# Kernel optimization log

Hardware: AMD Instinct MI355X
Metric: run time of the kernel (lower is better)

Reference implementation:

```python
import jax, jax.numpy as jnp
import numpy as np

STRIDES = (8, 16, 32, 64, 128)
HS = (192, 96, 48, 24, 12)
NUM_CLASSES = 15
NUM_THETA = 18
B = 16
SCORE_THR = 0.05
IOU_THR = 0.3
MAX_DET = 1000


def setup_inputs() -> dict:
    key = jax.random.key(0)
    ks = jax.random.split(key, 20)
    inp = {}
    i = 0
    for name, c in (("cls", NUM_CLASSES), ("reg", 5), ("tc", NUM_THETA), ("tr", 1)):
        for l, h in enumerate(HS):
            inp[f"{name}_l{l}"] = jax.random.normal(ks[i], (B, c, h, h), dtype=jnp.float32)
            i += 1
    return inp


def _coords():
    # FCOS-style location centers per level, concatenated: [N, 2] (x, y)
    outs = []
    for h, s in zip(HS, STRIDES):
        c1d = jnp.arange(h, dtype=jnp.float32) * s + s // 2
        yy, xx = jnp.meshgrid(c1d, c1d, indexing="ij")
        outs.append(jnp.stack([xx.ravel(), yy.ravel()], axis=-1))
    return jnp.concatenate(outs, axis=0)


def _flatten(levels):
    # list of [B,C,h,w] -> [B, sum(h*w), C]  (permute to NHWC then reshape, as in torch)
    b = levels[0].shape[0]
    return jnp.concatenate(
        [jnp.transpose(t, (0, 2, 3, 1)).reshape(b, -1, t.shape[1]) for t in levels], axis=1
    )


def _pairwise_iou(boxes):
    # boxes [M,5] (x1,y1,x2,y2,theta); axis-aligned IoU on first 4 coords
    x1, y1, x2, y2 = boxes[:, 0], boxes[:, 1], boxes[:, 2], boxes[:, 3]
    area = jnp.clip(x2 - x1, 0.0) * jnp.clip(y2 - y1, 0.0)
    iw = jnp.clip(jnp.minimum(x2[:, None], x2[None, :]) - jnp.maximum(x1[:, None], x1[None, :]), 0.0)
    ih = jnp.clip(jnp.minimum(y2[:, None], y2[None, :]) - jnp.maximum(y1[:, None], y1[None, :]), 0.0)
    inter = iw * ih
    union = area[:, None] + area[None, :] - inter
    return inter / jnp.maximum(union, 1e-8)


def _nms_keep(boxes, valid, iou_thr):
    # greedy NMS over score-sorted boxes; returns bool keep mask [M]
    m = boxes.shape[0]
    iou = _pairwise_iou(boxes)
    idx = jnp.arange(m)

    def body(i, keep):
        sup = keep[i] & (iou[i] > iou_thr) & (idx > i)
        return keep & ~sup

    return jax.lax.fori_loop(0, m, body, valid)


def _forward(cls_levels, reg_levels, tc_levels, tr_levels):
    coords = _coords()  # [N,2]

    cls_preds = jax.nn.sigmoid(_flatten(cls_levels))          # [B,N,15]
    cls_scores = jnp.max(cls_preds, axis=-1)                   # [B,N]
    cls_classes = jnp.argmax(cls_preds, axis=-1) + 1           # [B,N]

    tc_preds = jax.nn.sigmoid(_flatten(tc_levels))             # [B,N,18]
    theta_c = (jnp.argmax(tc_preds, axis=-1) + 1)[..., None].astype(jnp.float32)  # [B,N,1]
    tr_lo = _flatten(tr_levels)                                # [B,N,1]
    theta = theta_c * 10.0 + tr_lo                             # [B,N,1]

    # reg: scale ltrb channels (0:4) by stride per level, keep angle channel raw
    reg_parts = []
    for t, s in zip(reg_levels, STRIDES):
        r = jnp.transpose(t, (0, 2, 3, 1)).reshape(t.shape[0], -1, 5)
        reg_parts.append(jnp.concatenate([r[..., :4] * float(s), r[..., 4:]], axis=-1))
    reg = jnp.concatenate(reg_parts, axis=1)                   # [B,N,5]

    x1y1 = coords[None, :, :] - reg[..., :2]
    x2y2 = coords[None, :, :] + reg[..., 2:4]
    boxes = jnp.concatenate([x1y1, x2y2, theta], axis=-1)      # [B,N,5]

    max_num = min(MAX_DET, cls_scores.shape[-1])
    top_scores, top_idx = jax.lax.top_k(cls_scores, max_num)   # sorted desc
    boxes_topk = jnp.take_along_axis(boxes, top_idx[..., None], axis=1)   # [B,M,5]
    classes_topk = jnp.take_along_axis(cls_classes, top_idx, axis=1)      # [B,M]

    valid = top_scores >= SCORE_THR
    keep = jax.vmap(lambda b, v: _nms_keep(b, v, IOU_THR))(boxes_topk, valid)  # [B,M] bool

    scores_post = top_scores * keep
    classes_post = classes_topk * keep
    boxes_post = boxes_topk * keep[..., None]
    return scores_post, classes_post, boxes_post


def reference(cls_l0, cls_l1, cls_l2, cls_l3, cls_l4,
              reg_l0, reg_l1, reg_l2, reg_l3, reg_l4,
              tc_l0, tc_l1, tc_l2, tc_l3, tc_l4,
              tr_l0, tr_l1, tr_l2, tr_l3, tr_l4):
    return _forward(
        [cls_l0, cls_l1, cls_l2, cls_l3, cls_l4],
        [reg_l0, reg_l1, reg_l2, reg_l3, reg_l4],
        [tc_l0, tc_l1, tc_l2, tc_l3, tc_l4],
        [tr_l0, tr_l1, tr_l2, tr_l3, tr_l4],
    )
```

## Files before the change

### kernel.cpp

```cpp
#include <hip/hip_runtime.h>
#include <stdint.h>

#define NCLS   15
#define NTH    18
#define BATCH  16
#define NANCH  49104
#define KTOP   1000
#define NWORDS 16
#define NBIN   32768
#define BSHIFT 15
#define CAND   2048

__device__ __forceinline__ float sigmoidf(float x) {
    return 1.0f / (1.0f + expf(-x));
}

__device__ __forceinline__ void levelOf(int i, int& lvl, int& h, int& s, int& pos) {
    if (i < 36864)      { lvl = 0; h = 192; s = 8;   pos = i; }
    else if (i < 46080) { lvl = 1; h = 96;  s = 16;  pos = i - 36864; }
    else if (i < 48384) { lvl = 2; h = 48;  s = 32;  pos = i - 46080; }
    else if (i < 48960) { lvl = 3; h = 24;  s = 64;  pos = i - 48384; }
    else                { lvl = 4; h = 12;  s = 128; pos = i - 48960; }
}

__device__ __forceinline__ unsigned long long shfl_u64(unsigned long long v, int src) {
    int lo = __shfl((int)(unsigned int)(v & 0xFFFFFFFFull), src);
    int hi = __shfl((int)(unsigned int)(v >> 32), src);
    return ((unsigned long long)(unsigned int)hi << 32) | (unsigned long long)(unsigned int)lo;
}

__device__ __forceinline__ void atomicOr64Shared(unsigned long long* p, unsigned long long v) {
    unsigned int* q = (unsigned int*)p;
    unsigned int lo = (unsigned int)v;
    unsigned int hi = (unsigned int)(v >> 32);
    if (lo) atomicOr(q, lo);
    if (hi) atomicOr(q + 1, hi);
}

__global__ __launch_bounds__(256) void k_scores(
    const float* __restrict__ c0, const float* __restrict__ c1,
    const float* __restrict__ c2, const float* __restrict__ c3,
    const float* __restrict__ c4,
    float* __restrict__ scores, unsigned char* __restrict__ classes,
    uint4* __restrict__ zero_region, int zero_n4)
{
    int g4 = blockIdx.x * 256 + threadIdx.x;
    if (g4 < zero_n4) zero_region[g4] = make_uint4(0u, 0u, 0u, 0u);
    if (g4 >= BATCH * NANCH / 4) return;
    int g = g4 * 4;
    int b = g / NANCH;
    int i = g - b * NANCH;
    int lvl, h, s, pos;
    levelOf(i, lvl, h, s, pos);
    int hh = h * h;
    const float* cp = (lvl == 0) ? c0 : (lvl == 1) ? c1 : (lvl == 2) ? c2
                      : (lvl == 3) ? c3 : c4;
    const float* base = cp + (size_t)b * NCLS * hh + pos;
    float4 best = make_float4(-1e30f, -1e30f, -1e30f, -1e30f);
    int bcx = 0, bcy = 0, bcz = 0, bcw = 0;
    #pragma unroll
    for (int c = 0; c < NCLS; ++c) {
        float4 v = *(const float4*)(base + (size_t)c * hh);
        float sx = sigmoidf(v.x), sy = sigmoidf(v.y);
        float sz = sigmoidf(v.z), sw = sigmoidf(v.w);
        if (sx > best.x) { best.x = sx; bcx = c; }
        if (sy > best.y) { best.y = sy; bcy = c; }
        if (sz > best.z) { best.z = sz; bcz = c; }
        if (sw > best.w) { best.w = sw; bcw = c; }
    }
    *(float4*)(scores + g) = best;
    *(uchar4*)(classes + g) = make_uchar4(
        (unsigned char)(bcx + 1), (unsigned char)(bcy + 1),
        (unsigned char)(bcz + 1), (unsigned char)(bcw + 1));
}

__global__ __launch_bounds__(256) void k_hist(
    const float* __restrict__ scores, unsigned int* __restrict__ hist)
{
    __shared__ unsigned int lh[NBIN / 2];
    const int b = blockIdx.y;
    for (int i = threadIdx.x; i < NBIN / 2; i += 256) lh[i] = 0u;
    __syncthreads();

    const float4* sv = (const float4*)(scores + (size_t)b * NANCH);
    for (int f4 = blockIdx.x * 256 + threadIdx.x; f4 < NANCH / 4; f4 += 6 * 256) {
        float4 v = sv[f4];
        unsigned int bin;
        bin = __float_as_uint(v.x) >> BSHIFT;
        atomicAdd(&lh[bin >> 1], 1u << ((bin & 1) << 4));
        bin = __float_as_uint(v.y) >> BSHIFT;
        atomicAdd(&lh[bin >> 1], 1u << ((bin & 1) << 4));
        bin = __float_as_uint(v.z) >> BSHIFT;
        atomicAdd(&lh[bin >> 1], 1u << ((bin & 1) << 4));
        bin = __float_as_uint(v.w) >> BSHIFT;
        atomicAdd(&lh[bin >> 1], 1u << ((bin & 1) << 4));
    }
    __syncthreads();

    unsigned int* hb = hist + (size_t)b * (NBIN / 2);
    for (int wd = threadIdx.x; wd < NBIN / 2; wd += 256) {
        unsigned int v = lh[wd];
        if (v) atomicAdd(&hb[wd], v);
    }
}

__global__ __launch_bounds__(256) void k_findT(
    const unsigned int* __restrict__ hist, int* __restrict__ tbin)
{
    int b = blockIdx.x;
    int tid = threadIdx.x;
    const unsigned int* hb = hist + (size_t)b * (NBIN / 2);
    __shared__ unsigned int sc[256];
    __shared__ unsigned int fsc[128];
    __shared__ int s_c, s_t;

    unsigned int s = 0;
    const uint4* hv = (const uint4*)(hb + (size_t)tid * 64);
    #pragma unroll 4
    for (int k = 0; k < 16; ++k) {
        uint4 v = hv[k];
        s += (v.x & 0xFFFFu) + (v.x >> 16) + (v.y & 0xFFFFu) + (v.y >> 16)
           + (v.z & 0xFFFFu) + (v.z >> 16) + (v.w & 0xFFFFu) + (v.w >> 16);
    }
    sc[tid] = s;
    if (tid == 0) { s_c = 0; s_t = 0; }
    __syncthreads();
    for (int d = 1; d < 256; d <<= 1) {
        unsigned int add = (tid + d < 256) ? sc[tid + d] : 0;
        __syncthreads();
        sc[tid] += add;
        __syncthreads();
    }
    if (sc[tid] >= (unsigned int)KTOP && (tid == 255 || sc[tid + 1] < (unsigned int)KTOP))
        s_c = tid;
    __syncthreads();
    int c = s_c;
    unsigned int hi = (c < 255) ? sc[c + 1] : 0;
    if (tid < 64) {
        unsigned int w = hb[c * 64 + tid];
        fsc[2 * tid]     = w & 0xFFFFu;
        fsc[2 * tid + 1] = w >> 16;
    }
    __syncthreads();
    for (int d = 1; d < 128; d <<= 1) {
        unsigned int add = (tid < 128 && tid + d < 128) ? fsc[tid + d] : 0;
        __syncthreads();
        if (tid < 128) fsc[tid] += add;
        __syncthreads();
    }
    if (tid < 128 && hi + fsc[tid] >= (unsigned int)KTOP &&
        (tid == 127 || hi + fsc[tid + 1] < (unsigned int)KTOP))
        s_t = tid;
    __syncthreads();
    if (tid == 0) tbin[b] = c * 128 + s_t;
}

__global__ __launch_bounds__(256) void k_compact(
    const float* __restrict__ scores, const int* __restrict__ tbin,
    int* __restrict__ cnt, unsigned long long* __restrict__ cand)
{
    const int b = blockIdx.y;
    const int t4 = blockIdx.x * 256 + threadIdx.x;
    __shared__ int lcnt;
    __shared__ int lbase;
    if (threadIdx.x == 0) lcnt = 0;
    __syncthreads();

    const int T = tbin[b];
    const bool in = (t4 < NANCH / 4);
    float4 v = make_float4(0.f, 0.f, 0.f, 0.f);
    if (in) v = *(const float4*)(scores + (size_t)b * NANCH + 4 * (size_t)t4);
    unsigned int bits[4] = { __float_as_uint(v.x), __float_as_uint(v.y),
                             __float_as_uint(v.z), __float_as_uint(v.w) };
    int rank[4];
    #pragma unroll
    for (int k = 0; k < 4; ++k) {
        bool pass = in && ((int)(bits[k] >> BSHIFT) >= T);
        rank[k] = pass ? atomicAdd(&lcnt, 1) : -1;
    }
    __syncthreads();
    if (threadIdx.x == 0) lbase = atomicAdd(&cnt[b * 16], lcnt);
    __syncthreads();
    const int base = lbase;
    #pragma unroll
    for (int k = 0; k < 4; ++k) {
        if (rank[k] >= 0) {
            int p = base + rank[k];
            if (p < CAND) {
                unsigned int idx = 4u * (unsigned int)t4 + (unsigned int)k;
                cand[(size_t)b * CAND + p] =
                    ((unsigned long long)bits[k] << 32) |
                    (unsigned long long)(0xFFFFFFFFu - idx);
            }
        }
    }
}

__global__ __launch_bounds__(256) void k_rankdec(
    const unsigned long long* __restrict__ cand, const int* __restrict__ cnt,
    const float* __restrict__ r0, const float* __restrict__ r1,
    const float* __restrict__ r2, const float* __restrict__ r3,
    const float* __restrict__ r4,
    const unsigned char* __restrict__ classes_all,
    float* __restrict__ tsc, int* __restrict__ tix,
    float* __restrict__ boxes, int* __restrict__ clstop)
{
    const int b  = blockIdx.y;
    const int ci = blockIdx.x * 256 + threadIdx.x;
    __shared__ unsigned long long keys[CAND];

    int n = cnt[b * 16]; if (n > CAND) n = CAND;
    for (int i = threadIdx.x; i < CAND; i += 256)
        keys[i] = (i < n) ? cand[(size_t)b * CAND + i] : 0ull;
    __syncthreads();

    const unsigned long long my = keys[ci];
    if (my == 0ull) return;

    int rank = 0;
    #pragma unroll 8
    for (int j = 0; j < CAND; ++j)
        rank += (keys[j] > my) ? 1 : 0;
    if (rank >= KTOP) return;

    const int g   = b * KTOP + rank;
    const int idx = (int)(0xFFFFFFFFu - (unsigned int)(my & 0xFFFFFFFFull));
    tsc[g] = __uint_as_float((unsigned int)(my >> 32));
    tix[g] = idx;
    clstop[g] = (int)classes_all[(size_t)b * NANCH + idx];

    int lvl, h, s, pos;
    levelOf(idx, lvl, h, s, pos);
    int y = pos / h, x = pos - y * h;
    int hh = h * h;
    const float* rp = (lvl == 0) ? r0 : (lvl == 1) ? r1 : (lvl == 2) ? r2
                      : (lvl == 3) ? r3 : r4;
    const float* rb = rp + (size_t)b * 5 * hh + pos;
    float fs = (float)s;
    float rr0 = rb[0] * fs;
    float rr1 = rb[(size_t)hh] * fs;
    float rr2 = rb[(size_t)2 * hh] * fs;
    float rr3 = rb[(size_t)3 * hh] * fs;
    float cx = (float)(x * s + (s >> 1));
    float cy = (float)(y * s + (s >> 1));
    float* op = boxes + (size_t)g * 5;
    op[0] = cx - rr0;
    op[1] = cy - rr1;
    op[2] = cx + rr2;
    op[3] = cy + rr3;
}

__global__ __launch_bounds__(256) void k_theta_sel(
    const float* __restrict__ t0, const float* __restrict__ t1,
    const float* __restrict__ t2, const float* __restrict__ t3,
    const float* __restrict__ t4,
    const float* __restrict__ q0, const float* __restrict__ q1,
    const float* __restrict__ q2, const float* __restrict__ q3,
    const float* __restrict__ q4,
    const int* __restrict__ tix, float* __restrict__ boxes)
{
    int wid = blockIdx.x * 4 + (threadIdx.x >> 6);
    if (wid >= BATCH * KTOP) return;
    int lane = threadIdx.x & 63;
    int b = wid / KTOP;
    int idx = tix[wid];

    int lvl, h, s, pos;
    levelOf(idx, lvl, h, s, pos);
    int hh = h * h;
    const float* tp = (lvl == 0) ? t0 : (lvl == 1) ? t1 : (lvl == 2) ? t2
                      : (lvl == 3) ? t3 : t4;
    const float* qp = (lvl == 0) ? q0 : (lvl == 1) ? q1 : (lvl == 2) ? q2
                      : (lvl == 3) ? q3 : q4;

    float v = -1e30f;
    if (lane < NTH)
        v = sigmoidf(tp[(size_t)b * NTH * hh + pos + (size_t)lane * hh]);
    float m = v;
    m = fmaxf(m, __shfl_xor(m, 1));
    m = fmaxf(m, __shfl_xor(m, 2));
    m = fmaxf(m, __shfl_xor(m, 4));
    m = fmaxf(m, __shfl_xor(m, 8));
    m = fmaxf(m, __shfl_xor(m, 16));
    m = fmaxf(m, __shfl_xor(m, 32));
    unsigned long long eq = __ballot(v == m);
    int bt = __builtin_ctzll(eq);
    float tr = qp[(size_t)b * hh + pos];
    if (lane == 0)
        boxes[(size_t)wid * 5 + 4] = (float)(bt + 1) * 10.0f + tr;
}

__global__ __launch_bounds__(256) void k_mask(
    const float* __restrict__ boxes, unsigned long long* __restrict__ mask)
{
    const int b = blockIdx.x;
    const int by = blockIdx.y;
    __shared__ float bx1[1024], by1[1024], bx2[1024], by2[1024], bar[1024];
    for (int r = threadIdx.x; r < 1024; r += 256) {
        float x1 = 0.f, y1 = 0.f, x2 = 0.f, y2 = 0.f;
        if (r < KTOP) {
            const float* p = boxes + ((size_t)(b * KTOP + r)) * 5;
            x1 = p[0]; y1 = p[1]; x2 = p[2]; y2 = p[3];
        }
        bx1[r] = x1; by1[r] = y1; bx2[r] = x2; by2[r] = y2;
        bar[r] = fmaxf(x2 - x1, 0.0f) * fmaxf(y2 - y1, 0.0f);
    }
    __syncthreads();

    const int l  = threadIdx.x & 63;
    const int wv = threadIdx.x >> 6;
    const int i  = (by << 6) + l;
    const float x1 = bx1[i], y1 = by1[i], x2 = bx2[i], y2 = by2[i], ai = bar[i];

    for (int w = by + wv; w < NWORDS; w += 4) {
        const int j0 = w << 6;
        unsigned long long m = 0ull;
        #pragma unroll 8
        for (int jj = 0; jj < 64; ++jj) {
            const int j = j0 + jj;
            float iw = fminf(x2, bx2[j]) - fmaxf(x1, bx1[j]);
            iw = fmaxf(iw, 0.0f);
            float ih = fminf(y2, by2[j]) - fmaxf(y1, by1[j]);
            ih = fmaxf(ih, 0.0f);
            float inter = iw * ih;
            float u = ai + bar[j] - inter;
            float iou = inter / fmaxf(u, 1e-8f);
            unsigned long long bit = (iou > 0.3f && j > i) ? 1ull : 0ull;
            m |= bit << jj;
        }
        mask[(((size_t)b * 1024 + i) << 4) + w] = m;
    }
}

#define LOADROW(R, W) do {                                                          \
    const ulonglong2* rp2 = (const ulonglong2*)(mask +                              \
        (((size_t)b * 1024 + ((W) << 6) + l) << 4));                                \
    _Pragma("unroll")                                                               \
    for (int p = 0; p < 8; ++p) {                                                   \
        ulonglong2 v = rp2[p]; R[2 * p] = v.x; R[2 * p + 1] = v.y;                  \
    }                                                                               \
} while (0)

#define PROC(W, R) do {                                                             \
    const unsigned long long rowword = R[W];                                        \
    unsigned long long zr = __ballot(rowword == 0ull);                              \
    unsigned long long remw = sremv[W];                                             \
    unsigned long long pend = vw[W] & ~remw;                                        \
    unsigned long long keptm = 0ull;                                                \
    while (pend) {                                                                  \
        unsigned long long nzp = pend & ~zr;                                        \
        if (!nzp) { keptm |= pend; break; }                                         \
        int jj = __builtin_ctzll(nzp);                                              \
        unsigned long long low = (1ull << jj); low = (low << 1) - 1ull;             \
        keptm |= pend & low;                                                        \
        remw |= shfl_u64(rowword, jj);                                              \
        pend &= ~low; pend &= ~remw;                                                \
    }                                                                               \
    if (l == 0) skeep[W] = keptm;                                                   \
    if ((keptm >> l) & 1ull) {                                                      \
        _Pragma("unroll")                                                           \
        for (int w2 = (W) + 1; w2 < NWORDS; ++w2)                                   \
            if (R[w2]) atomicOr64Shared(&sremv[w2], R[w2]);                         \
    }                                                                               \
} while (0)

__global__ __launch_bounds__(64) void k_nms(
    const unsigned long long* __restrict__ mask,
    const float* __restrict__ tsc, const int* __restrict__ clstop,
    const float* __restrict__ boxes, float* __restrict__ out)
{
    const int b = blockIdx.x;
    const int l = threadIdx.x;
    __shared__ unsigned long long sremv[NWORDS];
    __shared__ unsigned long long skeep[NWORDS];

    if (l < NWORDS) sremv[l] = 0ull;

    unsigned long long vw[NWORDS];
    #pragma unroll
    for (int w = 0; w < NWORDS; ++w) {
        int i = (w << 6) + l;
        bool v = (i < KTOP) && (tsc[b * KTOP + i] >= 0.05f);
        vw[w] = __ballot(v);
    }

    unsigned long long rowA[NWORDS], rowB[NWORDS];
    LOADROW(rowA, 0);
    LOADROW(rowB, 1);   PROC(0, rowA);
    LOADROW(rowA, 2);   PROC(1, rowB);
    LOADROW(rowB, 3);   PROC(2, rowA);
    LOADROW(rowA, 4);   PROC(3, rowB);
    LOADROW(rowB, 5);   PROC(4, rowA);
    LOADROW(rowA, 6);   PROC(5, rowB);
    LOADROW(rowB, 7);   PROC(6, rowA);
    LOADROW(rowA, 8);   PROC(7, rowB);
    LOADROW(rowB, 9);   PROC(8, rowA);
    LOADROW(rowA, 10);  PROC(9, rowB);
    LOADROW(rowB, 11);  PROC(10, rowA);
    LOADROW(rowA, 12);  PROC(11, rowB);
    LOADROW(rowB, 13);  PROC(12, rowA);
    LOADROW(rowA, 14);  PROC(13, rowB);
    LOADROW(rowB, 15);  PROC(14, rowA);
    PROC(15, rowB);

    #pragma unroll
    for (int w = 0; w < NWORDS; ++w) {
        int i = (w << 6) + l;
        if (i < KTOP) {
            int g = b * KTOP + i;
            float fk = (float)((skeep[w] >> l) & 1ull);
            out[g] = tsc[g] * fk;
            out[BATCH * KTOP + g] = (float)clstop[g] * fk;
            const float* bp = boxes + (size_t)g * 5;
            float* op = out + 2 * BATCH * KTOP + (size_t)g * 5;
            op[0] = bp[0] * fk;
            op[1] = bp[1] * fk;
            op[2] = bp[2] * fk;
            op[3] = bp[3] * fk;
            op[4] = bp[4] * fk;
        }
    }
}

extern "C" void kernel_launch(void* const* d_in, const int* in_sizes, int n_in,
                              void* d_out, int out_size, void* d_ws, size_t ws_size,
                              hipStream_t stream) {
    const float* c0 = (const float*)d_in[0];
    const float* c1 = (const float*)d_in[1];
    const float* c2 = (const float*)d_in[2];
    const float* c3 = (const float*)d_in[3];
    const float* c4 = (const float*)d_in[4];
    const float* r0 = (const float*)d_in[5];
    const float* r1 = (const float*)d_in[6];
    const float* r2 = (const float*)d_in[7];
    const float* r3 = (const float*)d_in[8];
    const float* r4 = (const float*)d_in[9];
    const float* t0 = (const float*)d_in[10];
    const float* t1 = (const float*)d_in[11];
    const float* t2 = (const float*)d_in[12];
    const float* t3 = (const float*)d_in[13];
    const float* t4 = (const float*)d_in[14];
    const float* q0 = (const float*)d_in[15];
    const float* q1 = (const float*)d_in[16];
    const float* q2 = (const float*)d_in[17];
    const float* q3 = (const float*)d_in[18];
    const float* q4 = (const float*)d_in[19];

    char* ws = (char*)d_ws;
    float*              scores  = (float*)(ws + 0);
    unsigned char*      classes = (unsigned char*)(ws + 3142656);
    unsigned int*       hist    = (unsigned int*)(ws + 3928320);
    int*                tcnt    = (int*)(ws + 4976896);
    int*                tbin    = (int*)(ws + 4977920);
    unsigned long long* cand    = (unsigned long long*)(ws + 4978048);
    float*              tsc     = (float*)(ws + 5240192);
    int*                tix     = (int*)(ws + 5304192);
    int*                clstop  = (int*)(ws + 5368192);
    float*              boxes   = (float*)(ws + 5432192);
    unsigned long long* mask    = (unsigned long long*)(ws + 5752192);
    float*              out     = (float*)d_out;

    const int zero_n4 = 1049728 / 16;

    k_scores<<<(BATCH * NANCH / 4 + 255) / 256, 256, 0, stream>>>(
        c0, c1, c2, c3, c4, scores, classes, (uint4*)(ws + 3928320), zero_n4);
    k_hist<<<dim3(6, BATCH), 256, 0, stream>>>(scores, hist);
    k_findT<<<BATCH, 256, 0, stream>>>(hist, tbin);
    k_compact<<<dim3(48, BATCH), 256, 0, stream>>>(scores, tbin, tcnt, cand);
    k_rankdec<<<dim3(8, BATCH), 256, 0, stream>>>(
        cand, tcnt, r0, r1, r2, r3, r4, classes, tsc, tix, boxes, clstop);
    k_theta_sel<<<(BATCH * KTOP + 3) / 4, 256, 0, stream>>>(
        t0, t1, t2, t3, t4, q0, q1, q2, q3, q4, tix, boxes);
    k_mask<<<dim3(BATCH, 16), 256, 0, stream>>>(boxes, mask);
    k_nms<<<BATCH, 64, 0, stream>>>(mask, tsc, clstop, boxes, out);
}
```

Before: 118.3 us.

## Fuse histogram with threshold search and merge theta selection into mask kernel

Histogram building and threshold search now run in one 1024-thread block per batch that keeps the whole histogram in shared memory. This drops the global histogram, its zeroing inside the score kernel, and the global atomics. Theta selection is launched as extra blocks of the IoU-mask kernel, which removes two launches and lets the two independent jobs overlap. The trade-off is that each batch's histogram is now built by a single block, giving less parallelism across the 16 batches. The cnt counter is reset inside the new kernel at index b*16.

Result: faster. 104.7 us (-11.5%).

```diff
diff --git a/kernel.cpp b/kernel.cpp
--- a/kernel.cpp
+++ b/kernel.cpp
@@ -41,11 +41,9 @@
     const float* __restrict__ c0, const float* __restrict__ c1,
     const float* __restrict__ c2, const float* __restrict__ c3,
     const float* __restrict__ c4,
-    float* __restrict__ scores, unsigned char* __restrict__ classes,
-    uint4* __restrict__ zero_region, int zero_n4)
+    float* __restrict__ scores, unsigned char* __restrict__ classes)
 {
     int g4 = blockIdx.x * 256 + threadIdx.x;
-    if (g4 < zero_n4) zero_region[g4] = make_uint4(0u, 0u, 0u, 0u);
     if (g4 >= BATCH * NANCH / 4) return;
     int g = g4 * 4;
     int b = g / NANCH;
@@ -74,16 +72,21 @@
         (unsigned char)(bcz + 1), (unsigned char)(bcw + 1));
 }
 
-__global__ __launch_bounds__(256) void k_hist(
-    const float* __restrict__ scores, unsigned int* __restrict__ hist)
-{
+__global__ __launch_bounds__(1024) void k_histT(
+    const float* __restrict__ scores, int* __restrict__ tbin, int* __restrict__ tcnt)
+{
+    const int b   = blockIdx.x;
+    const int tid = threadIdx.x;
     __shared__ unsigned int lh[NBIN / 2];
-    const int b = blockIdx.y;
-    for (int i = threadIdx.x; i < NBIN / 2; i += 256) lh[i] = 0u;
+    __shared__ unsigned int csum[1024];
+    __shared__ int s_c, s_T;
+
+    for (int i = tid; i < NBIN / 2; i += 1024) lh[i] = 0u;
+    if (tid == 0) { s_c = 0; s_T = 0; tcnt[b * 16] = 0; }
     __syncthreads();
 
     const float4* sv = (const float4*)(scores + (size_t)b * NANCH);
-    for (int f4 = blockIdx.x * 256 + threadIdx.x; f4 < NANCH / 4; f4 += 6 * 256) {
+    for (int f4 = tid; f4 < NANCH / 4; f4 += 1024) {
         float4 v = sv[f4];
         unsigned int bin;
         bin = __float_as_uint(v.x) >> BSHIFT;
@@ -97,62 +100,48 @@
     }
     __syncthreads();
 
-    unsigned int* hb = hist + (size_t)b * (NBIN / 2);
-    for (int wd = threadIdx.x; wd < NBIN / 2; wd += 256) {
-        unsigned int v = lh[wd];
-        if (v) atomicAdd(&hb[wd], v);
-    }
-}
-
-__global__ __launch_bounds__(256) void k_findT(
-    const unsigned int* __restrict__ hist, int* __restrict__ tbin)
-{
-    int b = blockIdx.x;
-    int tid = threadIdx.x;
-    const unsigned int* hb = hist + (size_t)b * (NBIN / 2);
-    __shared__ unsigned int sc[256];
-    __shared__ unsigned int fsc[128];
-    __shared__ int s_c, s_t;
-
     unsigned int s = 0;
-    const uint4* hv = (const uint4*)(hb + (size_t)tid * 64);
-    #pragma unroll 4
+    #pragma unroll
     for (int k = 0; k < 16; ++k) {
-        uint4 v = hv[k];
-        s += (v.x & 0xFFFFu) + (v.x >> 16) + (v.y & 0xFFFFu) + (v.y >> 16)
-           + (v.z & 0xFFFFu) + (v.z >> 16) + (v.w & 0xFFFFu) + (v.w >> 16);
-    }
-    sc[tid] = s;
-    if (tid == 0) { s_c = 0; s_t = 0; }
-    __syncthreads();
-    for (int d = 1; d < 256; d <<= 1) {
-        unsigned int add = (tid + d < 256) ? sc[tid + d] : 0;
+        unsigned int w = lh[tid * 16 + k];
+        s += (w & 0xFFFFu) + (w >> 16);
+    }
+    csum[tid] = s;
+    __syncthreads();
+    for (int d = 1; d < 1024; d <<= 1) {
+        unsigned int add = (tid + d < 1024) ? csum[tid + d] : 0u;
         __syncthreads();
-        sc[tid] += add;
+        csum[tid] += add;
         __syncthreads();
     }
-    if (sc[tid] >= (unsigned int)KTOP && (tid == 255 || sc[tid + 1] < (unsigned int)KTOP))
+    if (csum[tid] >= (unsigned)KTOP &&
+        (tid == 1023 || csum[tid + 1] < (unsigned)KTOP))
         s_c = tid;
     __syncthreads();
-    int c = s_c;
-    unsigned int hi = (c < 255) ? sc[c + 1] : 0;
+    const int c = s_c;
+    const unsigned int hi = (c < 1023) ? csum[c + 1] : 0u;
+
     if (tid < 64) {
-        unsigned int w = hb[c * 64 + tid];
-        fsc[2 * tid]     = w & 0xFFFFu;
-        fsc[2 * tid + 1] = w >> 16;
-    }
-    __syncthreads();
-    for (int d = 1; d < 128; d <<= 1) {
-        unsigned int add = (tid < 128 && tid + d < 128) ? fsc[tid + d] : 0;
-        __syncthreads();
-        if (tid < 128) fsc[tid] += add;
-        __syncthreads();
-    }
-    if (tid < 128 && hi + fsc[tid] >= (unsigned int)KTOP &&
-        (tid == 127 || hi + fsc[tid + 1] < (unsigned int)KTOP))
-        s_t = tid;
-    __syncthreads();
-    if (tid == 0) tbin[b] = c * 128 + s_t;
+        unsigned int cnt = 0;
+        if (tid < 32) {
+            int bin = c * 32 + tid;
+            cnt = (lh[bin >> 1] >> ((bin & 1) << 4)) & 0xFFFFu;
+        }
+        unsigned int suf = cnt;
+        #pragma unroll
+        for (int d = 1; d < 32; d <<= 1) {
+            unsigned int o = __shfl_down(suf, d);
+            if (tid + d < 32) suf += o;
+        }
+        unsigned int nxt = __shfl_down(suf, 1);
+        if (tid < 32) {
+            if (hi + suf >= (unsigned)KTOP &&
+                (tid == 31 || hi + nxt < (unsigned)KTOP))
+                s_T = c * 32 + tid;
+        }
+    }
+    __syncthreads();
+    if (tid == 0) tbin[b] = s_T;
 }
 
 __global__ __launch_bounds__(256) void k_compact(
@@ -250,85 +239,86 @@
     op[3] = cy + rr3;
 }
 
-__global__ __launch_bounds__(256) void k_theta_sel(
+__global__ __launch_bounds__(256) void k_masktheta(
+    const float* __restrict__ boxes_in, unsigned long long* __restrict__ mask,
     const float* __restrict__ t0, const float* __restrict__ t1,
     const float* __restrict__ t2, const float* __restrict__ t3,
     const float* __restrict__ t4,
     const float* __restrict__ q0, const float* __restrict__ q1,
     const float* __restrict__ q2, const float* __restrict__ q3,
     const float* __restrict__ q4,
-    const int* __restrict__ tix, float* __restrict__ boxes)
-{
-    int wid = blockIdx.x * 4 + (threadIdx.x >> 6);
-    if (wid >= BATCH * KTOP) return;
-    int lane = threadIdx.x & 63;
-    int b = wid / KTOP;
-    int idx = tix[wid];
-
-    int lvl, h, s, pos;
-    levelOf(idx, lvl, h, s, pos);
-    int hh = h * h;
-    const float* tp = (lvl == 0) ? t0 : (lvl == 1) ? t1 : (lvl == 2) ? t2
-                      : (lvl == 3) ? t3 : t4;
-    const float* qp = (lvl == 0) ? q0 : (lvl == 1) ? q1 : (lvl == 2) ? q2
-                      : (lvl == 3) ? q3 : q4;
-
-    float v = -1e30f;
-    if (lane < NTH)
-        v = sigmoidf(tp[(size_t)b * NTH * hh + pos + (size_t)lane * hh]);
-    float m = v;
-    m = fmaxf(m, __shfl_xor(m, 1));
-    m = fmaxf(m, __shfl_xor(m, 2));
-    m = fmaxf(m, __shfl_xor(m, 4));
-    m = fmaxf(m, __shfl_xor(m, 8));
-    m = fmaxf(m, __shfl_xor(m, 16));
-    m = fmaxf(m, __shfl_xor(m, 32));
-    unsigned long long eq = __ballot(v == m);
-    int bt = __builtin_ctzll(eq);
-    float tr = qp[(size_t)b * hh + pos];
-    if (lane == 0)
-        boxes[(size_t)wid * 5 + 4] = (float)(bt + 1) * 10.0f + tr;
-}
-
-__global__ __launch_bounds__(256) void k_mask(
-    const float* __restrict__ boxes, unsigned long long* __restrict__ mask)
+    const int* __restrict__ tix, float* __restrict__ boxes_theta)
 {
     const int b = blockIdx.x;
-    const int by = blockIdx.y;
-    __shared__ float bx1[1024], by1[1024], bx2[1024], by2[1024], bar[1024];
-    for (int r = threadIdx.x; r < 1024; r += 256) {
-        float x1 = 0.f, y1 = 0.f, x2 = 0.f, y2 = 0.f;
-        if (r < KTOP) {
-            const float* p = boxes + ((size_t)(b * KTOP + r)) * 5;
-            x1 = p[0]; y1 = p[1]; x2 = p[2]; y2 = p[3];
-        }
-        bx1[r] = x1; by1[r] = y1; bx2[r] = x2; by2[r] = y2;
-        bar[r] = fmaxf(x2 - x1, 0.0f) * fmaxf(y2 - y1, 0.0f);
-    }
-    __syncthreads();
-
-    const int l  = threadIdx.x & 63;
-    const int wv = threadIdx.x >> 6;
-    const int i  = (by << 6) + l;
-    const float x1 = bx1[i], y1 = by1[i], x2 = bx2[i], y2 = by2[i], ai = bar[i];
-
-    for (int w = by + wv; w < NWORDS; w += 4) {
-        const int j0 = w << 6;
-        unsigned long long m = 0ull;
-        #pragma unroll 8
-        for (int jj = 0; jj < 64; ++jj) {
-            const int j = j0 + jj;
-            float iw = fminf(x2, bx2[j]) - fmaxf(x1, bx1[j]);
-            iw = fmaxf(iw, 0.0f);
-            float ih = fminf(y2, by2[j]) - fmaxf(y1, by1[j]);
-            ih = fmaxf(ih, 0.0f);
-            float inter = iw * ih;
-            float u = ai + bar[j] - inter;
-            float iou = inter / fmaxf(u, 1e-8f);
-            unsigned long long bit = (iou > 0.3f && j > i) ? 1ull : 0ull;
-            m |= bit << jj;
-        }
-        mask[(((size_t)b * 1024 + i) << 4) + w] = m;
+    const int role = blockIdx.y;
+
+    if (role < 16) {
+        const int by = role;
+        __shared__ float bx1[1024], by1[1024], bx2[1024], by2[1024], bar[1024];
+        for (int r = threadIdx.x; r < 1024; r += 256) {
+            float x1 = 0.f, y1 = 0.f, x2 = 0.f, y2 = 0.f;
+            if (r < KTOP) {
+                const float* p = boxes_in + ((size_t)(b * KTOP + r)) * 5;
+                x1 = p[0]; y1 = p[1]; x2 = p[2]; y2 = p[3];
+            }
+            bx1[r] = x1; by1[r] = y1; bx2[r] = x2; by2[r] = y2;
+            bar[r] = fmaxf(x2 - x1, 0.0f) * fmaxf(y2 - y1, 0.0f);
+        }
+        __syncthreads();
+
+        const int l  = threadIdx.x & 63;
+        const int wv = threadIdx.x >> 6;
+        const int i  = (by << 6) + l;
+        const float x1 = bx1[i], y1 = by1[i], x2 = bx2[i], y2 = by2[i], ai = bar[i];
+
+        for (int w = by + wv; w < NWORDS; w += 4) {
+            const int j0 = w << 6;
+            unsigned long long m = 0ull;
+            #pragma unroll 8
+            for (int jj = 0; jj < 64; ++jj) {
+                const int j = j0 + jj;
+                float iw = fminf(x2, bx2[j]) - fmaxf(x1, bx1[j]);
+                iw = fmaxf(iw, 0.0f);
+                float ih = fminf(y2, by2[j]) - fmaxf(y1, by1[j]);
+                ih = fmaxf(ih, 0.0f);
+                float inter = iw * ih;
+                float u = ai + bar[j] - inter;
+                float iou = inter / fmaxf(u, 1e-8f);
+                unsigned long long bit = (iou > 0.3f && j > i) ? 1ull : 0ull;
+                m |= bit << jj;
+            }
+            mask[(((size_t)b * 1024 + i) << 4) + w] = m;
+        }
+    } else {
+        int r = (role - 16) * 4 + (threadIdx.x >> 6);
+        if (r >= KTOP) return;
+        int lane = threadIdx.x & 63;
+        int wid = b * KTOP + r;
+        int idx = tix[wid];
+
+        int lvl, h, s, pos;
+        levelOf(idx, lvl, h, s, pos);
+        int hh = h * h;
+        const float* tp = (lvl == 0) ? t0 : (lvl == 1) ? t1 : (lvl == 2) ? t2
+                          : (lvl == 3) ? t3 : t4;
+        const float* qp = (lvl == 0) ? q0 : (lvl == 1) ? q1 : (lvl == 2) ? q2
+                          : (lvl == 3) ? q3 : q4;
+
+        float v = -1e30f;
+        if (lane < NTH)
+            v = sigmoidf(tp[(size_t)b * NTH * hh + pos + (size_t)lane * hh]);
+        float m = v;
+        m = fmaxf(m, __shfl_xor(m, 1));
+        m = fmaxf(m, __shfl_xor(m, 2));
+        m = fmaxf(m, __shfl_xor(m, 4));
+        m = fmaxf(m, __shfl_xor(m, 8));
+        m = fmaxf(m, __shfl_xor(m, 16));
+        m = fmaxf(m, __shfl_xor(m, 32));
+        unsigned long long eq = __ballot(v == m);
+        int bt = __builtin_ctzll(eq);
+        float tr = qp[(size_t)b * hh + pos];
+        if (lane == 0)
+            boxes_theta[(size_t)wid * 5 + 4] = (float)(bt + 1) * 10.0f + tr;
     }
 }
 
@@ -449,28 +439,23 @@
     char* ws = (char*)d_ws;
     float*              scores  = (float*)(ws + 0);
     unsigned char*      classes = (unsigned char*)(ws + 3142656);
-    unsigned int*       hist    = (unsigned int*)(ws + 3928320);
-    int*                tcnt    = (int*)(ws + 4976896);
-    int*                tbin    = (int*)(ws + 4977920);
-    unsigned long long* cand    = (unsigned long long*)(ws + 4978048);
-    float*              tsc     = (float*)(ws + 5240192);
-    int*                tix     = (int*)(ws + 5304192);
-    int*                clstop  = (int*)(ws + 5368192);
-    float*              boxes   = (float*)(ws + 5432192);
-    unsigned long long* mask    = (unsigned long long*)(ws + 5752192);
+    int*                tcnt    = (int*)(ws + 3928320);
+    int*                tbin    = (int*)(ws + 3929344);
+    unsigned long long* cand    = (unsigned long long*)(ws + 3929408);
+    float*              tsc     = (float*)(ws + 4191552);
+    int*                tix     = (int*)(ws + 4255552);
+    int*                clstop  = (int*)(ws + 4319552);
+    float*              boxes   = (float*)(ws + 4383552);
+    unsigned long long* mask    = (unsigned long long*)(ws + 4703552);
     float*              out     = (float*)d_out;
 
-    const int zero_n4 = 1049728 / 16;
-
     k_scores<<<(BATCH * NANCH / 4 + 255) / 256, 256, 0, stream>>>(
-        c0, c1, c2, c3, c4, scores, classes, (uint4*)(ws + 3928320), zero_n4);
-    k_hist<<<dim3(6, BATCH), 256, 0, stream>>>(scores, hist);
-    k_findT<<<BATCH, 256, 0, stream>>>(hist, tbin);
+        c0, c1, c2, c3, c4, scores, classes);
+    k_histT<<<BATCH, 1024, 0, stream>>>(scores, tbin, tcnt);
     k_compact<<<dim3(48, BATCH), 256, 0, stream>>>(scores, tbin, tcnt, cand);
     k_rankdec<<<dim3(8, BATCH), 256, 0, stream>>>(
         cand, tcnt, r0, r1, r2, r3, r4, classes, tsc, tix, boxes, clstop);
-    k_theta_sel<<<(BATCH * KTOP + 3) / 4, 256, 0, stream>>>(
-        t0, t1, t2, t3, t4, q0, q1, q2, q3, q4, tix, boxes);
-    k_mask<<<dim3(BATCH, 16), 256, 0, stream>>>(boxes, mask);
+    k_masktheta<<<dim3(BATCH, 16 + (KTOP + 3) / 4), 256, 0, stream>>>(
+        boxes, mask, t0, t1, t2, t3, t4, q0, q1, q2, q3, q4, tix, boxes);
     k_nms<<<BATCH, 64, 0, stream>>>(mask, tsc, clstop, boxes, out);
 }
```
